# Kernel tuning notes

Hardware: AMD Instinct MI355X
Metric: run time of the kernel (lower is better)

The kernel has to match this reference:

```python
import jax, jax.numpy as jnp
import numpy as np
import math

DIM = 1024
MAX_SEQ_LEN = 8192

def setup_inputs() -> dict:
    key = jax.random.key(0)
    k1, k2, k3, k4 = jax.random.split(key, 4)
    x = jax.random.normal(k1, (4, 4096, DIM), dtype=jnp.float32)
    base_phases = jax.random.normal(k2, (MAX_SEQ_LEN, DIM), dtype=jnp.float32) * math.pi
    # nn.Linear(dim, dim): weight [out, in], bias [out]
    bound = 1.0 / math.sqrt(DIM)
    W = jax.random.uniform(k3, (DIM, DIM), dtype=jnp.float32, minval=-bound, maxval=bound)
    b = jax.random.uniform(k4, (DIM,), dtype=jnp.float32, minval=-bound, maxval=bound)
    return {"x": x, "base_phases": base_phases, "W": W, "b": b}

def reference(x, base_phases, W, b):
    B, L, D = x.shape
    phases = base_phases[:L][None, :, :]          # [1, L, D]
    value = jnp.einsum('bld,ed->ble', x, W) + b   # Linear: x @ W.T + b
    cos_p = jnp.cos(phases)
    sin_p = jnp.sin(phases)
    mem_real = jnp.cumsum(value * cos_p, axis=1)
    mem_imag = jnp.cumsum(value * sin_p, axis=1)
    retrieved = mem_real * cos_p + mem_imag * sin_p
    positions = jnp.arange(1, L + 1, dtype=jnp.float32)
    norm = jnp.sqrt(positions)[None, :, None]     # [1, L, 1]
    return retrieved / norm
```

## Files before the change

### kernel.cpp

```cpp
#include <hip/hip_runtime.h>
#include <hip/hip_bf16.h>

#define DIM 1024
#define SEQ 4096
#define NB 4
#define MROWS (NB * SEQ)
#define NC 64
#define CL (SEQ / NC)

#define BM 256
#define BN 256
#define BK 32
#define NT (DIM / BK)
#define TILE_LDS 32768
#define GEMM_LDS (4 * TILE_LDS)

typedef __attribute__((ext_vector_type(8))) short bf16x8;
typedef __attribute__((ext_vector_type(4))) float f32x4;

static __device__ __forceinline__ unsigned short f2bf(float f) {
    union { float f; unsigned u; } v; v.f = f;
    unsigned r = v.u + 0x7FFF + ((v.u >> 16) & 1);
    return (unsigned short)(r >> 16);
}

static __device__ __forceinline__ float bf2f(unsigned short h) {
    union { unsigned u; float f; } v; v.u = ((unsigned)h) << 16;
    return v.f;
}

static __device__ __forceinline__ unsigned int bfpair(float a, float b) {
    unsigned ua = __float_as_uint(a), ub = __float_as_uint(b);
    unsigned ra = (ua + 0x7FFF + ((ua >> 16) & 1)) >> 16;
    unsigned rb = (ub + 0x7FFF + ((ub >> 16) & 1)) & 0xFFFF0000u;
    return ra | rb;
}
static __device__ __forceinline__ uint4 packbf8(float4 lo, float4 hi) {
    uint4 r;
    r.x = bfpair(lo.x, lo.y); r.y = bfpair(lo.z, lo.w);
    r.z = bfpair(hi.x, hi.y); r.w = bfpair(hi.z, hi.w);
    return r;
}

static __device__ __forceinline__ void gload_lds16(const void* g, void* l) {
    __builtin_amdgcn_global_load_lds((const __attribute__((address_space(1))) void*)g,
                                     (__attribute__((address_space(3))) void*)l, 16, 0, 0);
}

__global__ void convertW_kernel(const float* __restrict__ W, unsigned short* __restrict__ wb) {
    int t = blockIdx.x * 256 + threadIdx.x;
    float4 v = ((const float4*)W)[t];
    ushort4 o;
    o.x = f2bf(v.x); o.y = f2bf(v.y); o.z = f2bf(v.z); o.w = f2bf(v.w);
    ((ushort4*)wb)[t] = o;
}

static __device__ __forceinline__ void stage_B(const unsigned short* __restrict__ Bm, char* smem,
                                               int q, int n0, int ks, int w, int lane) {
    const int c16 = (lane & 3) ^ ((lane >> 3) & 3);
#pragma unroll
    for (int r = 0; r < 2; ++r) {
        int row = r * 128 + w * 16 + (lane >> 2);
        const unsigned short* g = Bm + (size_t)(n0 + row) * DIM + ks + c16 * 8;
        char* l = smem + q * TILE_LDS + 16384 + (r * 128 + w * 16) * 64 + lane * 16;
        gload_lds16(g, l);
    }
}

__global__ __launch_bounds__(512, 2) void gemm_kernel(const float* __restrict__ X,
                                                      const unsigned short* __restrict__ Bm,
                                                      const float* __restrict__ bias,
                                                      unsigned short* __restrict__ V) {
    extern __shared__ char smem[];
    const int tid  = threadIdx.x;
    const int lane = tid & 63;
    const int w    = tid >> 6;
    const int wm   = w >> 2;
    const int wn   = w & 3;
    const int wr   = wm * 128;
    const int wc   = wn * 64;
    const int rl   = lane & 15;
    const int rh   = lane >> 4;
    const int swz  = (rh ^ ((rl >> 1) & 3)) * 16;
    const int m0   = blockIdx.x * BM;
    const int n0   = blockIdx.y * BN;
    const int c16  = (lane & 3) ^ ((lane >> 3) & 3);
    const int arow = w * 16 + (lane >> 2);
    const size_t dstA = (size_t)(w * 16) * 64 + (size_t)lane * 16;

    f32x4 acc[8][4];
#pragma unroll
    for (int m = 0; m < 8; ++m)
#pragma unroll
        for (int n = 0; n < 4; ++n)
            acc[m][n] = (f32x4){0.f, 0.f, 0.f, 0.f};

    float bv[4];
#pragma unroll
    for (int nf = 0; nf < 4; ++nf)
        bv[nf] = bias[n0 + wc + nf * 16 + rl];

    const float* Xa = X + (size_t)(m0 + arow) * DIM + c16 * 8;
    const float* Xb = X + (size_t)(m0 + 128 + arow) * DIM + c16 * 8;

    float4 aCl0, aCh0, aCl1, aCh1;
    float4 aNl0, aNh0, aNl1, aNh1;

    {
        aCl0 = *(const float4*)(Xa + 0); aCh0 = *(const float4*)(Xa + 4);
        aCl1 = *(const float4*)(Xb + 0); aCh1 = *(const float4*)(Xb + 4);
        *(uint4*)(smem + 0 * TILE_LDS + dstA)             = packbf8(aCl0, aCh0);
        *(uint4*)(smem + 0 * TILE_LDS + 128 * 64 + dstA)  = packbf8(aCl1, aCh1);
        stage_B(Bm, smem, 0, n0, 0, w, lane);
        aCl0 = *(const float4*)(Xa + BK); aCh0 = *(const float4*)(Xa + BK + 4);
        aCl1 = *(const float4*)(Xb + BK); aCh1 = *(const float4*)(Xb + BK + 4);
        *(uint4*)(smem + 1 * TILE_LDS + dstA)             = packbf8(aCl0, aCh0);
        *(uint4*)(smem + 1 * TILE_LDS + 128 * 64 + dstA)  = packbf8(aCl1, aCh1);
        stage_B(Bm, smem, 1, n0, BK, w, lane);
        aCl0 = *(const float4*)(Xa + 2 * BK); aCh0 = *(const float4*)(Xa + 2 * BK + 4);
        aCl1 = *(const float4*)(Xb + 2 * BK); aCh1 = *(const float4*)(Xb + 2 * BK + 4);
    }
    asm volatile("s_waitcnt lgkmcnt(0)" ::: "memory");
    __builtin_amdgcn_s_barrier();

#pragma unroll 4
    for (int t = 0; t < NT; ++t) {
        const int q   = t & 3;
        const int qw  = (t + 2) & 3;
        const int ksB = ((t + 2) & (NT - 1)) * BK;
        const int ksA = ((t + 3) & (NT - 1)) * BK;
        char* base = smem + q * TILE_LDS;

        stage_B(Bm, smem, qw, n0, ksB, w, lane);
        aNl0 = *(const float4*)(Xa + ksA); aNh0 = *(const float4*)(Xa + ksA + 4);
        aNl1 = *(const float4*)(Xb + ksA); aNh1 = *(const float4*)(Xb + ksA + 4);

        bf16x8 bfr[4];
#pragma unroll
        for (int nf = 0; nf < 4; ++nf)
            bfr[nf] = *(const bf16x8*)(base + 16384 + (wc + nf * 16 + rl) * 64 + swz);
        bf16x8 af[4];
#pragma unroll
        for (int mf = 0; mf < 4; ++mf)
            af[mf] = *(const bf16x8*)(base + (wr + mf * 16 + rl) * 64 + swz);
        __builtin_amdgcn_s_setprio(1);
#pragma unroll
        for (int mf = 0; mf < 4; ++mf)
#pragma unroll
            for (int nf = 0; nf < 4; ++nf)
                acc[mf][nf] = __builtin_amdgcn_mfma_f32_16x16x32_bf16(af[mf], bfr[nf], acc[mf][nf], 0, 0, 0);
        __builtin_amdgcn_s_setprio(0);

        *(uint4*)(smem + qw * TILE_LDS + dstA)            = packbf8(aCl0, aCh0);
        *(uint4*)(smem + qw * TILE_LDS + 128 * 64 + dstA) = packbf8(aCl1, aCh1);

#pragma unroll
        for (int mf = 0; mf < 4; ++mf)
            af[mf] = *(const bf16x8*)(base + (wr + (mf + 4) * 16 + rl) * 64 + swz);
        __builtin_amdgcn_s_setprio(1);
#pragma unroll
        for (int mf = 0; mf < 4; ++mf)
#pragma unroll
            for (int nf = 0; nf < 4; ++nf)
                acc[mf + 4][nf] = __builtin_amdgcn_mfma_f32_16x16x32_bf16(af[mf], bfr[nf], acc[mf + 4][nf], 0, 0, 0);
        __builtin_amdgcn_s_setprio(0);

        aCl0 = aNl0; aCh0 = aNh0; aCl1 = aNl1; aCh1 = aNh1;

        asm volatile("s_waitcnt vmcnt(6)" ::: "memory");
        asm volatile("s_waitcnt lgkmcnt(0)" ::: "memory");
        __builtin_amdgcn_sched_barrier(0);
        __builtin_amdgcn_s_barrier();
    }

#pragma unroll
    for (int mf = 0; mf < 8; ++mf) {
#pragma unroll
        for (int nf = 0; nf < 4; ++nf) {
            int gcol = n0 + wc + nf * 16 + rl;
#pragma unroll
            for (int j = 0; j < 4; ++j) {
                int grow = m0 + wr + mf * 16 + rh * 4 + j;
                V[(size_t)grow * DIM + gcol] = f2bf(acc[mf][nf][j] + bv[nf]);
            }
        }
    }
}

__global__ void passA_kernel(const unsigned short* __restrict__ val, const float* __restrict__ ph,
                             float* __restrict__ pr, float* __restrict__ pi) {
    int t  = blockIdx.x * 256 + threadIdx.x;
    int c  = blockIdx.y;
    int bb = blockIdx.z;
    const ushort2* v = (const ushort2*)val + ((size_t)bb * SEQ + (size_t)c * CL) * (DIM / 2) + t;
    const float2*  p = (const float2*)ph + (size_t)c * CL * (DIM / 2) + t;
    float sr0 = 0.f, si0 = 0.f, sr1 = 0.f, si1 = 0.f;
    for (int l = 0; l < CL; ++l) {
        ushort2 vv = v[(size_t)l * (DIM / 2)];
        float2  pp = p[(size_t)l * (DIM / 2)];
        float v0 = bf2f(vv.x), v1 = bf2f(vv.y);
        float s0, c0, s1, c1;
        __sincosf(pp.x, &s0, &c0);
        __sincosf(pp.y, &s1, &c1);
        sr0 += v0 * c0; si0 += v0 * s0;
        sr1 += v1 * c1; si1 += v1 * s1;
    }
    size_t idx = ((size_t)bb * NC + c) * DIM + 2 * t;
    pr[idx] = sr0; pr[idx + 1] = sr1;
    pi[idx] = si0; pi[idx + 1] = si1;
}

__global__ void passB_kernel(float* __restrict__ pr, float* __restrict__ pi) {
    int t = blockIdx.x * 256 + threadIdx.x;
    int bb = t >> 10;
    int e  = t & 1023;
    float r = 0.f, im = 0.f;
    for (int c = 0; c < NC; ++c) {
        size_t idx = ((size_t)bb * NC + c) * DIM + e;
        float tr = pr[idx], ti = pi[idx];
        pr[idx] = r; pi[idx] = im;
        r += tr; im += ti;
    }
}

__global__ void passC_kernel(const unsigned short* __restrict__ val, const float* __restrict__ ph,
                             const float* __restrict__ pr, const float* __restrict__ pi,
                             float* __restrict__ out) {
    int t  = blockIdx.x * 256 + threadIdx.x;
    int c  = blockIdx.y;
    int bb = blockIdx.z;
    size_t base = ((size_t)bb * SEQ + (size_t)c * CL) * (DIM / 2) + t;
    const ushort2* v = (const ushort2*)val + base;
    const float2*  p = (const float2*)ph + (size_t)c * CL * (DIM / 2) + t;
    float2* o = (float2*)out + base;
    size_t pidx = ((size_t)bb * NC + c) * DIM + 2 * t;
    float ar0 = pr[pidx], ar1 = pr[pidx + 1];
    float ai0 = pi[pidx], ai1 = pi[pidx + 1];
    const int l0 = c * CL;
    for (int l = 0; l < CL; ++l) {
        ushort2 vv = v[(size_t)l * (DIM / 2)];
        float2  pp = p[(size_t)l * (DIM / 2)];
        float v0 = bf2f(vv.x), v1 = bf2f(vv.y);
        float s0, c0, s1, c1;
        __sincosf(pp.x, &s0, &c0);
        __sincosf(pp.y, &s1, &c1);
        ar0 += v0 * c0; ai0 += v0 * s0;
        ar1 += v1 * c1; ai1 += v1 * s1;
        float rn = rsqrtf((float)(l0 + l + 1));
        float2 ov;
        ov.x = (ar0 * c0 + ai0 * s0) * rn;
        ov.y = (ar1 * c1 + ai1 * s1) * rn;
        o[(size_t)l * (DIM / 2)] = ov;
    }
}

extern "C" void kernel_launch(void* const* d_in, const int* in_sizes, int n_in,
                              void* d_out, int out_size, void* d_ws, size_t ws_size,
                              hipStream_t stream) {
    const float* x  = (const float*)d_in[0];
    const float* ph = (const float*)d_in[1];
    const float* W  = (const float*)d_in[2];
    const float* b  = (const float*)d_in[3];
    float* out = (float*)d_out;

    unsigned short* vb = (unsigned short*)d_ws;
    unsigned short* wb = vb + (size_t)MROWS * DIM;
    float* pr = (float*)(wb + (size_t)DIM * DIM);
    float* pi = pr + (size_t)NB * NC * DIM;

    (void)hipFuncSetAttribute((const void*)gemm_kernel,
                              hipFuncAttributeMaxDynamicSharedMemorySize, GEMM_LDS);

    convertW_kernel<<<DIM * DIM / 4 / 256, 256, 0, stream>>>(W, wb);
    {
        dim3 grid(MROWS / BM, DIM / BN);
        gemm_kernel<<<grid, 512, GEMM_LDS, stream>>>(x, wb, b, vb);
    }
    {
        dim3 grid(DIM / 512, NC, NB);
        passA_kernel<<<grid, 256, 0, stream>>>(vb, ph, pr, pi);
    }
    passB_kernel<<<16, 256, 0, stream>>>(pr, pi);
    {
        dim3 grid(DIM / 512, NC, NB);
        passC_kernel<<<grid, 256, 0, stream>>>(vb, ph, pr, pi, out);
    }
}
```

Measured before the change: 90.33 us.

## Stage fp32 A tiles directly to LDS and convert at fragment load

The GEMM now streams fp32 X tiles into LDS with global_load_lds in a 3-slot ring, instead of loading into registers and packing to bf16 before LDS stores. It converts to bf16 with v_cvt_pk_bf16_f32 when reading fragments. It also swaps the MFMA operand order so each lane owns a row, which allows vectorized ushort4 output stores with float4 bias loads. This removes register round-trips and VGPR pressure from A staging but doubles A's LDS footprint and repeats the conversion work per wave.

```diff
diff --git a/kernel.cpp b/kernel.cpp
--- a/kernel.cpp
+++ b/kernel.cpp
@@ -11,9 +11,9 @@
 #define BM 256
 #define BN 256
 #define BK 32
-#define NT (DIM / BK)
-#define TILE_LDS 32768
-#define GEMM_LDS (4 * TILE_LDS)
+#define NTK 32
+#define SLOTB 49152
+#define GEMM_LDS (3 * SLOTB)
 
 typedef __attribute__((ext_vector_type(8))) short bf16x8;
 typedef __attribute__((ext_vector_type(4))) float f32x4;
@@ -29,16 +29,9 @@
     return v.f;
 }
 
-static __device__ __forceinline__ unsigned int bfpair(float a, float b) {
-    unsigned ua = __float_as_uint(a), ub = __float_as_uint(b);
-    unsigned ra = (ua + 0x7FFF + ((ua >> 16) & 1)) >> 16;
-    unsigned rb = (ub + 0x7FFF + ((ub >> 16) & 1)) & 0xFFFF0000u;
-    return ra | rb;
-}
-static __device__ __forceinline__ uint4 packbf8(float4 lo, float4 hi) {
-    uint4 r;
-    r.x = bfpair(lo.x, lo.y); r.y = bfpair(lo.z, lo.w);
-    r.z = bfpair(hi.x, hi.y); r.w = bfpair(hi.z, hi.w);
+static __device__ __forceinline__ unsigned cvtpk(float a, float b) {
+    unsigned r;
+    asm("v_cvt_pk_bf16_f32 %0, %1, %2" : "=v"(r) : "v"(a), "v"(b));
     return r;
 }
 
@@ -55,14 +48,22 @@
     ((ushort4*)wb)[t] = o;
 }
 
-static __device__ __forceinline__ void stage_B(const unsigned short* __restrict__ Bm, char* smem,
-                                               int q, int n0, int ks, int w, int lane) {
-    const int c16 = (lane & 3) ^ ((lane >> 3) & 3);
+static __device__ __forceinline__ void stage_Af32(const float* __restrict__ srcBase, char* smem,
+                                                  int slot, int kt, int w, int lane) {
+#pragma unroll
+    for (int j = 0; j < 4; ++j) {
+        const float* g = srcBase + (size_t)j * 8 * DIM + kt * BK;
+        char* l = smem + (size_t)slot * SLOTB + (w * 4 + j) * 1024 + lane * 16;
+        gload_lds16(g, l);
+    }
+}
+
+static __device__ __forceinline__ void stage_B16(const unsigned short* __restrict__ srcBase, char* smem,
+                                                 int slot, int kt, int w, int lane) {
 #pragma unroll
     for (int r = 0; r < 2; ++r) {
-        int row = r * 128 + w * 16 + (lane >> 2);
-        const unsigned short* g = Bm + (size_t)(n0 + row) * DIM + ks + c16 * 8;
-        char* l = smem + q * TILE_LDS + 16384 + (r * 128 + w * 16) * 64 + lane * 16;
+        const unsigned short* g = srcBase + (size_t)r * 128 * DIM + kt * BK;
+        char* l = smem + (size_t)slot * SLOTB + 32768 + (r * 128 + w * 16) * 64 + lane * 16;
         gload_lds16(g, l);
     }
 }
@@ -75,18 +76,20 @@
     const int tid  = threadIdx.x;
     const int lane = tid & 63;
     const int w    = tid >> 6;
-    const int wm   = w >> 2;
-    const int wn   = w & 3;
-    const int wr   = wm * 128;
-    const int wc   = wn * 64;
+    const int wr   = (w >> 2) * 128;
+    const int wc   = (w & 3) * 64;
     const int rl   = lane & 15;
     const int rh   = lane >> 4;
-    const int swz  = (rh ^ ((rl >> 1) & 3)) * 16;
     const int m0   = blockIdx.x * BM;
     const int n0   = blockIdx.y * BN;
-    const int c16  = (lane & 3) ^ ((lane >> 3) & 3);
-    const int arow = w * 16 + (lane >> 2);
-    const size_t dstA = (size_t)(w * 16) * 64 + (size_t)lane * 16;
+
+    const float* srcA = X + (size_t)(m0 + w * 32 + (lane >> 3)) * DIM + ((lane & 7) ^ (lane >> 3)) * 4;
+    const unsigned short* srcB = Bm + (size_t)(n0 + w * 16 + (lane >> 2)) * DIM
+                               + (((lane & 3) ^ ((lane >> 3) & 3)) * 8);
+
+    const int swzB = (rh ^ ((rl >> 1) & 3)) * 16;
+    const int aoff0 = (wr + rl) * 128 + (((rh * 2 + 0) ^ (rl & 7)) * 16);
+    const int aoff1 = (wr + rl) * 128 + (((rh * 2 + 1) ^ (rl & 7)) * 16);
 
     f32x4 acc[8][4];
 #pragma unroll
@@ -95,94 +98,80 @@
         for (int n = 0; n < 4; ++n)
             acc[m][n] = (f32x4){0.f, 0.f, 0.f, 0.f};
 
-    float bv[4];
+    float4 bv4[4];
 #pragma unroll
     for (int nf = 0; nf < 4; ++nf)
-        bv[nf] = bias[n0 + wc + nf * 16 + rl];
-
-    const float* Xa = X + (size_t)(m0 + arow) * DIM + c16 * 8;
-    const float* Xb = X + (size_t)(m0 + 128 + arow) * DIM + c16 * 8;
-
-    float4 aCl0, aCh0, aCl1, aCh1;
-    float4 aNl0, aNh0, aNl1, aNh1;
-
-    {
-        aCl0 = *(const float4*)(Xa + 0); aCh0 = *(const float4*)(Xa + 4);
-        aCl1 = *(const float4*)(Xb + 0); aCh1 = *(const float4*)(Xb + 4);
-        *(uint4*)(smem + 0 * TILE_LDS + dstA)             = packbf8(aCl0, aCh0);
-        *(uint4*)(smem + 0 * TILE_LDS + 128 * 64 + dstA)  = packbf8(aCl1, aCh1);
-        stage_B(Bm, smem, 0, n0, 0, w, lane);
-        aCl0 = *(const float4*)(Xa + BK); aCh0 = *(const float4*)(Xa + BK + 4);
-        aCl1 = *(const float4*)(Xb + BK); aCh1 = *(const float4*)(Xb + BK + 4);
-        *(uint4*)(smem + 1 * TILE_LDS + dstA)             = packbf8(aCl0, aCh0);
-        *(uint4*)(smem + 1 * TILE_LDS + 128 * 64 + dstA)  = packbf8(aCl1, aCh1);
-        stage_B(Bm, smem, 1, n0, BK, w, lane);
-        aCl0 = *(const float4*)(Xa + 2 * BK); aCh0 = *(const float4*)(Xa + 2 * BK + 4);
-        aCl1 = *(const float4*)(Xb + 2 * BK); aCh1 = *(const float4*)(Xb + 2 * BK + 4);
-    }
-    asm volatile("s_waitcnt lgkmcnt(0)" ::: "memory");
-    __builtin_amdgcn_s_barrier();
-
-#pragma unroll 4
-    for (int t = 0; t < NT; ++t) {
-        const int q   = t & 3;
-        const int qw  = (t + 2) & 3;
-        const int ksB = ((t + 2) & (NT - 1)) * BK;
-        const int ksA = ((t + 3) & (NT - 1)) * BK;
-        char* base = smem + q * TILE_LDS;
-
-        stage_B(Bm, smem, qw, n0, ksB, w, lane);
-        aNl0 = *(const float4*)(Xa + ksA); aNh0 = *(const float4*)(Xa + ksA + 4);
-        aNl1 = *(const float4*)(Xb + ksA); aNh1 = *(const float4*)(Xb + ksA + 4);
+        bv4[nf] = *(const float4*)(bias + n0 + wc + nf * 16 + rh * 4);
+
+    stage_Af32(srcA, smem, 0, 0, w, lane);
+    stage_B16 (srcB, smem, 0, 0, w, lane);
+    stage_Af32(srcA, smem, 1, 1, w, lane);
+    stage_B16 (srcB, smem, 1, 1, w, lane);
+
+#pragma unroll 1
+    for (int t = 0; t < NTK; ++t) {
+        asm volatile("s_waitcnt vmcnt(6)" ::: "memory");
+        __builtin_amdgcn_s_barrier();
+        const int sc = t % 3;
+        const int ss = (t + 2) % 3;
+        const int kn = (t + 2) & (NTK - 1);
+        const char* sb = smem + (size_t)sc * SLOTB;
 
         bf16x8 bfr[4];
 #pragma unroll
         for (int nf = 0; nf < 4; ++nf)
-            bfr[nf] = *(const bf16x8*)(base + 16384 + (wc + nf * 16 + rl) * 64 + swz);
+            bfr[nf] = *(const bf16x8*)(sb + 32768 + (wc + nf * 16 + rl) * 64 + swzB);
+
         bf16x8 af[4];
 #pragma unroll
+        for (int mf = 0; mf < 4; ++mf) {
+            f32x4 q0 = *(const f32x4*)(sb + mf * 2048 + aoff0);
+            f32x4 q1 = *(const f32x4*)(sb + mf * 2048 + aoff1);
+            union { unsigned u[4]; bf16x8 v; } cv;
+            cv.u[0] = cvtpk(q0[0], q0[1]); cv.u[1] = cvtpk(q0[2], q0[3]);
+            cv.u[2] = cvtpk(q1[0], q1[1]); cv.u[3] = cvtpk(q1[2], q1[3]);
+            af[mf] = cv.v;
+        }
+        stage_Af32(srcA, smem, ss, kn, w, lane);
+        __builtin_amdgcn_s_setprio(1);
+#pragma unroll
         for (int mf = 0; mf < 4; ++mf)
-            af[mf] = *(const bf16x8*)(base + (wr + mf * 16 + rl) * 64 + swz);
+#pragma unroll
+            for (int nf = 0; nf < 4; ++nf)
+                acc[mf][nf] = __builtin_amdgcn_mfma_f32_16x16x32_bf16(bfr[nf], af[mf], acc[mf][nf], 0, 0, 0);
+        __builtin_amdgcn_s_setprio(0);
+
+#pragma unroll
+        for (int mf = 0; mf < 4; ++mf) {
+            f32x4 q0 = *(const f32x4*)(sb + (mf + 4) * 2048 + aoff0);
+            f32x4 q1 = *(const f32x4*)(sb + (mf + 4) * 2048 + aoff1);
+            union { unsigned u[4]; bf16x8 v; } cv;
+            cv.u[0] = cvtpk(q0[0], q0[1]); cv.u[1] = cvtpk(q0[2], q0[3]);
+            cv.u[2] = cvtpk(q1[0], q1[1]); cv.u[3] = cvtpk(q1[2], q1[3]);
+            af[mf] = cv.v;
+        }
+        stage_B16(srcB, smem, ss, kn, w, lane);
         __builtin_amdgcn_s_setprio(1);
 #pragma unroll
         for (int mf = 0; mf < 4; ++mf)
 #pragma unroll
             for (int nf = 0; nf < 4; ++nf)
-                acc[mf][nf] = __builtin_amdgcn_mfma_f32_16x16x32_bf16(af[mf], bfr[nf], acc[mf][nf], 0, 0, 0);
+                acc[mf + 4][nf] = __builtin_amdgcn_mfma_f32_16x16x32_bf16(bfr[nf], af[mf], acc[mf + 4][nf], 0, 0, 0);
         __builtin_amdgcn_s_setprio(0);
-
-        *(uint4*)(smem + qw * TILE_LDS + dstA)            = packbf8(aCl0, aCh0);
-        *(uint4*)(smem + qw * TILE_LDS + 128 * 64 + dstA) = packbf8(aCl1, aCh1);
-
-#pragma unroll
-        for (int mf = 0; mf < 4; ++mf)
-            af[mf] = *(const bf16x8*)(base + (wr + (mf + 4) * 16 + rl) * 64 + swz);
-        __builtin_amdgcn_s_setprio(1);
-#pragma unroll
-        for (int mf = 0; mf < 4; ++mf)
-#pragma unroll
-            for (int nf = 0; nf < 4; ++nf)
-                acc[mf + 4][nf] = __builtin_amdgcn_mfma_f32_16x16x32_bf16(af[mf], bfr[nf], acc[mf + 4][nf], 0, 0, 0);
-        __builtin_amdgcn_s_setprio(0);
-
-        aCl0 = aNl0; aCh0 = aNh0; aCl1 = aNl1; aCh1 = aNh1;
-
-        asm volatile("s_waitcnt vmcnt(6)" ::: "memory");
-        asm volatile("s_waitcnt lgkmcnt(0)" ::: "memory");
-        __builtin_amdgcn_sched_barrier(0);
-        __builtin_amdgcn_s_barrier();
     }
 
 #pragma unroll
     for (int mf = 0; mf < 8; ++mf) {
+        int grow = m0 + wr + mf * 16 + rl;
 #pragma unroll
         for (int nf = 0; nf < 4; ++nf) {
-            int gcol = n0 + wc + nf * 16 + rl;
-#pragma unroll
-            for (int j = 0; j < 4; ++j) {
-                int grow = m0 + wr + mf * 16 + rh * 4 + j;
-                V[(size_t)grow * DIM + gcol] = f2bf(acc[mf][nf][j] + bv[nf]);
-            }
+            int gcol0 = n0 + wc + nf * 16 + rh * 4;
+            ushort4 o;
+            o.x = f2bf(acc[mf][nf][0] + bv4[nf].x);
+            o.y = f2bf(acc[mf][nf][1] + bv4[nf].y);
+            o.z = f2bf(acc[mf][nf][2] + bv4[nf].z);
+            o.w = f2bf(acc[mf][nf][3] + bv4[nf].w);
+            *(ushort4*)(V + (size_t)grow * DIM + gcol0) = o;
         }
     }
 }
```

After: 88.59 us. No clear change (-1.9%).
